# Optimization experiments

Hardware: AMD Instinct MI355X
Metric: run time of the kernel (lower is better)

Reference implementation:

```python
import jax, jax.numpy as jnp
import numpy as np

WS = 11
SIGMA = 1.5
CH = 3
C1 = (0.01 * 255.0) ** 2  # 6.5025
C2 = (0.03 * 255.0) ** 2  # 58.5225


def _gauss_window():
    # 1D Gaussian -> outer product -> depthwise kernel [C, 1, ws, ws] (OIHW)
    coords = jnp.arange(WS, dtype=jnp.float32) - WS // 2
    g = jnp.exp(-coords ** 2 / (2.0 * SIGMA ** 2))
    g = g / g.sum()
    w2d = g[:, None] * g[None, :]
    return jnp.tile(w2d[None, None], (CH, 1, 1, 1))


def _dwconv(x, win):
    pad = WS // 2
    return jax.lax.conv_general_dilated(
        x, win, window_strides=(1, 1), padding=[(pad, pad), (pad, pad)],
        feature_group_count=CH,
        dimension_numbers=('NCHW', 'OIHW', 'NCHW'))


def setup_inputs() -> dict:
    key = jax.random.key(0)
    k1, k2 = jax.random.split(key)
    shape = (32, 3, 512, 512)
    img_gen = jax.random.uniform(k1, shape, jnp.float32, -1.0, 1.0)
    img_ref = jax.random.uniform(k2, shape, jnp.float32, -1.0, 1.0)
    return {"img_gen": img_gen, "img_ref": img_ref}


def reference(img_gen, img_ref):
    gen = (img_gen + 1.0) * 0.5
    ref = (img_ref + 1.0) * 0.5
    win = _gauss_window()

    mu1 = _dwconv(gen, win)
    mu2 = _dwconv(ref, win)
    mu1_sq = mu1 * mu1
    mu2_sq = mu2 * mu2
    mu1_mu2 = mu1 * mu2
    sigma1_sq = _dwconv(gen * gen, win) - mu1_sq
    sigma2_sq = _dwconv(ref * ref, win) - mu2_sq
    sigma12 = _dwconv(gen * ref, win) - mu1_mu2

    ssim_map = ((2.0 * mu1_mu2 + C1) * (2.0 * sigma12 + C2)) / (
        (mu1_sq + mu2_sq + C1) * (sigma1_sq + sigma2_sq + C2))
    return 1.0 - ssim_map.mean()
```

## Files before the change

### kernel.cpp

```cpp
#include <hip/hip_runtime.h>

#define TX 64
#define TY 20
#define PROWS (TY + 10)
#define HSTR 67
#define IMW 512
#define IMH 512
#define NPLANES 96
#define NBX (IMW / TX)
#define NBY ((IMH + TY - 1) / TY)
#define NBLOCKS (NBX * NBY * NPLANES)

__device__ __forceinline__ float uniform_f(float v) {
  return __int_as_float(__builtin_amdgcn_readfirstlane(__float_as_int(v)));
}

__device__ __forceinline__ void gauss_weights(float* w) {
  double t[11];
  double s = 0.0;
#pragma unroll
  for (int i = 0; i < 11; ++i) {
    double d = (double)(i - 5);
    t[i] = exp(-d * d / 4.5);
    s += t[i];
  }
#pragma unroll
  for (int i = 0; i < 11; ++i) w[i] = uniform_f((float)(t[i] / s));
}

__global__ __launch_bounds__(256, 4) void ssim_main(
    const float* __restrict__ gen, const float* __restrict__ ref,
    float* __restrict__ partial) {
  __shared__ float sh[5][PROWS][HSTR];
  __shared__ float swsum[4];

  const int tid = threadIdx.x;
  const int bid = blockIdx.x;
  const int rem = bid % (NBX * NBY);
  const int plane = bid / (NBX * NBY);
  const int bx = rem % NBX;
  const int by = rem / NBX;
  const int x0 = bx * TX;
  const int y0 = by * TY;
  const float* gp = gen + (size_t)plane * (IMW * IMH);
  const float* rp = ref + (size_t)plane * (IMW * IMH);

  float w[11];
  gauss_weights(w);

  if (tid < PROWS * 8) {
    const int row = tid >> 3;
    const int xs = (tid & 7) * 8;
    const int gy = y0 - 5 + row;
    const bool rowok = (gy >= 0) && (gy < IMH);
    const int xbase = x0 + xs - 8;
    const float* grow = gp + (size_t)gy * IMW;
    const float* rrow = rp + (size_t)gy * IMW;

    float ga[24], ra[24];
#pragma unroll
    for (int k = 0; k < 6; ++k) {
      const int c = xbase + 4 * k;
      const bool ok = rowok && (c >= 0) && (c < IMW);
      float4 vg = make_float4(0.f, 0.f, 0.f, 0.f);
      float4 vr = make_float4(0.f, 0.f, 0.f, 0.f);
      if (ok) {
        float4 g4 = *(const float4*)(grow + c);
        float4 r4 = *(const float4*)(rrow + c);
        vg.x = fmaf(0.5f, g4.x, 0.5f); vg.y = fmaf(0.5f, g4.y, 0.5f);
        vg.z = fmaf(0.5f, g4.z, 0.5f); vg.w = fmaf(0.5f, g4.w, 0.5f);
        vr.x = fmaf(0.5f, r4.x, 0.5f); vr.y = fmaf(0.5f, r4.y, 0.5f);
        vr.z = fmaf(0.5f, r4.z, 0.5f); vr.w = fmaf(0.5f, r4.w, 0.5f);
      }
      ga[4 * k + 0] = vg.x; ga[4 * k + 1] = vg.y;
      ga[4 * k + 2] = vg.z; ga[4 * k + 3] = vg.w;
      ra[4 * k + 0] = vr.x; ra[4 * k + 1] = vr.y;
      ra[4 * k + 2] = vr.z; ra[4 * k + 3] = vr.w;
    }

    float acc[5][8];
#pragma unroll
    for (int q = 0; q < 5; ++q)
#pragma unroll
      for (int o = 0; o < 8; ++o) acc[q][o] = 0.f;

#pragma unroll
    for (int p = 0; p < 18; ++p) {
      const float g = ga[p + 3];
      const float r = ra[p + 3];
      const float gg = g * g;
      const float rr = r * r;
      const float gr = g * r;
      const int olo = (p - 10 < 0) ? 0 : p - 10;
      const int ohi = (p < 7) ? p : 7;
#pragma unroll
      for (int o = olo; o <= ohi; ++o) {
        const float wt = w[p - o];
        acc[0][o] = fmaf(wt, g, acc[0][o]);
        acc[1][o] = fmaf(wt, r, acc[1][o]);
        acc[2][o] = fmaf(wt, gg, acc[2][o]);
        acc[3][o] = fmaf(wt, rr, acc[3][o]);
        acc[4][o] = fmaf(wt, gr, acc[4][o]);
      }
    }
#pragma unroll
    for (int q = 0; q < 5; ++q)
#pragma unroll
      for (int o = 0; o < 8; ++o) sh[q][row][xs + o] = acc[q][o];
  }
  __syncthreads();

  const int col = tid & 63;
  const int r0 = (tid >> 6) * 5;
  float hv[5][15];
#pragma unroll
  for (int q = 0; q < 5; ++q)
#pragma unroll
    for (int i = 0; i < 15; ++i) hv[q][i] = sh[q][r0 + i][col];

  const float C1 = 6.5025f, C2 = 58.5225f;
  float lsum = 0.f;
#pragma unroll
  for (int o = 0; o < 5; ++o) {
    float mu1 = 0.f, mu2 = 0.f, e1 = 0.f, e2 = 0.f, e12 = 0.f;
#pragma unroll
    for (int t = 0; t < 11; ++t) {
      const float wt = w[t];
      mu1 = fmaf(wt, hv[0][o + t], mu1);
      mu2 = fmaf(wt, hv[1][o + t], mu2);
      e1 = fmaf(wt, hv[2][o + t], e1);
      e2 = fmaf(wt, hv[3][o + t], e2);
      e12 = fmaf(wt, hv[4][o + t], e12);
    }
    const float m12 = mu1 * mu2;
    const float m1s = mu1 * mu1;
    const float m2s = mu2 * mu2;
    const float num = (2.f * m12 + C1) * (2.f * (e12 - m12) + C2);
    const float den = (m1s + m2s + C1) * ((e1 - m1s) + (e2 - m2s) + C2);
    const int y = y0 + r0 + o;
    lsum += (y < IMH) ? (num / den) : 0.f;
  }

#pragma unroll
  for (int off = 32; off > 0; off >>= 1) lsum += __shfl_down(lsum, off, 64);
  if ((tid & 63) == 0) swsum[tid >> 6] = lsum;
  __syncthreads();
  if (tid == 0) partial[bid] = swsum[0] + swsum[1] + swsum[2] + swsum[3];
}

__global__ void ssim_reduce(const float* __restrict__ partial,
                            float* __restrict__ out) {
  const int nv = NBLOCKS / 4;
  double s = 0.0;
  for (int i = threadIdx.x; i < nv; i += 256) {
    float4 v = ((const float4*)partial)[i];
    s += (double)v.x + (double)v.y + (double)v.z + (double)v.w;
  }
#pragma unroll
  for (int off = 32; off > 0; off >>= 1) s += __shfl_down(s, off, 64);
  __shared__ double sd[4];
  if ((threadIdx.x & 63) == 0) sd[threadIdx.x >> 6] = s;
  __syncthreads();
  if (threadIdx.x == 0) {
    double npix = (double)NPLANES * (double)IMW * (double)IMH;
    out[0] = (float)(1.0 - (sd[0] + sd[1] + sd[2] + sd[3]) / npix);
  }
}

extern "C" void kernel_launch(void* const* d_in, const int* in_sizes, int n_in,
                              void* d_out, int out_size, void* d_ws, size_t ws_size,
                              hipStream_t stream) {
  (void)in_sizes; (void)n_in; (void)out_size; (void)ws_size;
  const float* gen = (const float*)d_in[0];
  const float* ref = (const float*)d_in[1];
  float* partial = (float*)d_ws;
  ssim_main<<<NBLOCKS, 256, 0, stream>>>(gen, ref, partial);
  ssim_reduce<<<1, 256, 0, stream>>>(partial, (float*)d_out);
}
```

Baseline: 310.5 us.

## Pack gen/ref channels into v_pk_fma_f32 and hardcode Gaussian weights

Pairs the gen and ref values (and their squares) into two-wide vectors and accumulates both blur passes with packed v_pk_fma_f32 inline asm, cutting the VALU instruction count for the separable convolution. It also hardcodes the Gaussian weights as constants instead of computing them in double precision per thread, adds a branch-free interior tile load path, reorganizes shared memory into interleaved float2 arrays written with float4 stores, and uses a fast divide. The risks are slightly different rounding from the fast divide and the constants, plus the inline asm limiting compiler scheduling. Out-of-bounds pixels now load -1 so they map to 0 after the affine transform.

```diff
diff --git a/kernel.cpp b/kernel.cpp
--- a/kernel.cpp
+++ b/kernel.cpp
@@ -1,9 +1,12 @@
 #include <hip/hip_runtime.h>
+
+typedef float v2f __attribute__((ext_vector_type(2)));
 
 #define TX 64
 #define TY 20
 #define PROWS (TY + 10)
-#define HSTR 67
+#define GRSTR 66
+#define SSTR 68
 #define IMW 512
 #define IMH 512
 #define NPLANES 96
@@ -11,28 +14,27 @@
 #define NBY ((IMH + TY - 1) / TY)
 #define NBLOCKS (NBX * NBY * NPLANES)
 
-__device__ __forceinline__ float uniform_f(float v) {
-  return __int_as_float(__builtin_amdgcn_readfirstlane(__float_as_int(v)));
-}
-
-__device__ __forceinline__ void gauss_weights(float* w) {
-  double t[11];
-  double s = 0.0;
-#pragma unroll
-  for (int i = 0; i < 11; ++i) {
-    double d = (double)(i - 5);
-    t[i] = exp(-d * d / 4.5);
-    s += t[i];
-  }
-#pragma unroll
-  for (int i = 0; i < 11; ++i) w[i] = uniform_f((float)(t[i] / s));
+#define GW0 0.00102838f
+#define GW1 0.00759877f
+#define GW2 0.03600077f
+#define GW3 0.10936069f
+#define GW4 0.21300553f
+#define GW5 0.26601172f
+
+__device__ __forceinline__ void pkfma(v2f& acc, v2f a, v2f b) {
+  asm("v_pk_fma_f32 %0, %1, %2, %0" : "+v"(acc) : "v"(a), "v"(b));
 }
 
 __global__ __launch_bounds__(256, 4) void ssim_main(
     const float* __restrict__ gen, const float* __restrict__ ref,
     float* __restrict__ partial) {
-  __shared__ float sh[5][PROWS][HSTR];
+  __shared__ __align__(16) v2f s_gr[PROWS][GRSTR];
+  __shared__ __align__(16) v2f s_qq[PROWS][GRSTR];
+  __shared__ __align__(16) float s_s[PROWS][SSTR];
   __shared__ float swsum[4];
+
+  const float GW[11] = {GW0, GW1, GW2, GW3, GW4, GW5,
+                        GW4, GW3, GW2, GW1, GW0};
 
   const int tid = threadIdx.x;
   const int bid = blockIdx.x;
@@ -45,100 +47,124 @@
   const float* gp = gen + (size_t)plane * (IMW * IMH);
   const float* rp = ref + (size_t)plane * (IMW * IMH);
 
-  float w[11];
-  gauss_weights(w);
-
   if (tid < PROWS * 8) {
     const int row = tid >> 3;
     const int xs = (tid & 7) * 8;
     const int gy = y0 - 5 + row;
-    const bool rowok = (gy >= 0) && (gy < IMH);
     const int xbase = x0 + xs - 8;
     const float* grow = gp + (size_t)gy * IMW;
     const float* rrow = rp + (size_t)gy * IMW;
 
-    float ga[24], ra[24];
-#pragma unroll
-    for (int k = 0; k < 6; ++k) {
-      const int c = xbase + 4 * k;
-      const bool ok = rowok && (c >= 0) && (c < IMW);
-      float4 vg = make_float4(0.f, 0.f, 0.f, 0.f);
-      float4 vr = make_float4(0.f, 0.f, 0.f, 0.f);
-      if (ok) {
-        float4 g4 = *(const float4*)(grow + c);
-        float4 r4 = *(const float4*)(rrow + c);
-        vg.x = fmaf(0.5f, g4.x, 0.5f); vg.y = fmaf(0.5f, g4.y, 0.5f);
-        vg.z = fmaf(0.5f, g4.z, 0.5f); vg.w = fmaf(0.5f, g4.w, 0.5f);
-        vr.x = fmaf(0.5f, r4.x, 0.5f); vr.y = fmaf(0.5f, r4.y, 0.5f);
-        vr.z = fmaf(0.5f, r4.z, 0.5f); vr.w = fmaf(0.5f, r4.w, 0.5f);
+    v2f P[24];
+    const bool interior = (bx >= 1) & (bx <= 6) & (by >= 1) & (by <= 24);
+    if (interior) {
+#pragma unroll
+      for (int k = 0; k < 6; ++k) {
+        const int c = xbase + 4 * k;
+        const float4 g4 = *(const float4*)(grow + c);
+        const float4 r4 = *(const float4*)(rrow + c);
+        P[4 * k + 0] = (v2f){fmaf(0.5f, g4.x, 0.5f), fmaf(0.5f, r4.x, 0.5f)};
+        P[4 * k + 1] = (v2f){fmaf(0.5f, g4.y, 0.5f), fmaf(0.5f, r4.y, 0.5f)};
+        P[4 * k + 2] = (v2f){fmaf(0.5f, g4.z, 0.5f), fmaf(0.5f, r4.z, 0.5f)};
+        P[4 * k + 3] = (v2f){fmaf(0.5f, g4.w, 0.5f), fmaf(0.5f, r4.w, 0.5f)};
       }
-      ga[4 * k + 0] = vg.x; ga[4 * k + 1] = vg.y;
-      ga[4 * k + 2] = vg.z; ga[4 * k + 3] = vg.w;
-      ra[4 * k + 0] = vr.x; ra[4 * k + 1] = vr.y;
-      ra[4 * k + 2] = vr.z; ra[4 * k + 3] = vr.w;
-    }
-
-    float acc[5][8];
-#pragma unroll
-    for (int q = 0; q < 5; ++q)
-#pragma unroll
-      for (int o = 0; o < 8; ++o) acc[q][o] = 0.f;
+    } else {
+      const bool rowok = (gy >= 0) && (gy < IMH);
+#pragma unroll
+      for (int k = 0; k < 6; ++k) {
+        const int c = xbase + 4 * k;
+        const bool ok = rowok && (c >= 0) && (c < IMW);
+        float4 g4 = make_float4(-1.f, -1.f, -1.f, -1.f);
+        float4 r4 = g4;
+        if (ok) {
+          g4 = *(const float4*)(grow + c);
+          r4 = *(const float4*)(rrow + c);
+        }
+        P[4 * k + 0] = (v2f){fmaf(0.5f, g4.x, 0.5f), fmaf(0.5f, r4.x, 0.5f)};
+        P[4 * k + 1] = (v2f){fmaf(0.5f, g4.y, 0.5f), fmaf(0.5f, r4.y, 0.5f)};
+        P[4 * k + 2] = (v2f){fmaf(0.5f, g4.z, 0.5f), fmaf(0.5f, r4.z, 0.5f)};
+        P[4 * k + 3] = (v2f){fmaf(0.5f, g4.w, 0.5f), fmaf(0.5f, r4.w, 0.5f)};
+      }
+    }
+
+    v2f accP[8], accQ[8];
+    float accS[8];
+#pragma unroll
+    for (int o = 0; o < 8; ++o) {
+      accP[o] = (v2f){0.f, 0.f};
+      accQ[o] = (v2f){0.f, 0.f};
+      accS[o] = 0.f;
+    }
 
 #pragma unroll
     for (int p = 0; p < 18; ++p) {
-      const float g = ga[p + 3];
-      const float r = ra[p + 3];
-      const float gg = g * g;
-      const float rr = r * r;
-      const float gr = g * r;
+      const v2f pv = P[p + 3];
+      v2f qv;
+      qv.x = pv.x * pv.x;
+      qv.y = pv.y * pv.y;
+      const float sv = pv.x * pv.y;
       const int olo = (p - 10 < 0) ? 0 : p - 10;
       const int ohi = (p < 7) ? p : 7;
 #pragma unroll
       for (int o = olo; o <= ohi; ++o) {
-        const float wt = w[p - o];
-        acc[0][o] = fmaf(wt, g, acc[0][o]);
-        acc[1][o] = fmaf(wt, r, acc[1][o]);
-        acc[2][o] = fmaf(wt, gg, acc[2][o]);
-        acc[3][o] = fmaf(wt, rr, acc[3][o]);
-        acc[4][o] = fmaf(wt, gr, acc[4][o]);
+        const float wt = GW[p - o];
+        const v2f wv = (v2f){wt, wt};
+        pkfma(accP[o], wv, pv);
+        pkfma(accQ[o], wv, qv);
+        accS[o] = fmaf(wt, sv, accS[o]);
       }
     }
-#pragma unroll
-    for (int q = 0; q < 5; ++q)
-#pragma unroll
-      for (int o = 0; o < 8; ++o) sh[q][row][xs + o] = acc[q][o];
+
+    float4* wp = (float4*)&s_gr[row][xs];
+    wp[0] = make_float4(accP[0].x, accP[0].y, accP[1].x, accP[1].y);
+    wp[1] = make_float4(accP[2].x, accP[2].y, accP[3].x, accP[3].y);
+    wp[2] = make_float4(accP[4].x, accP[4].y, accP[5].x, accP[5].y);
+    wp[3] = make_float4(accP[6].x, accP[6].y, accP[7].x, accP[7].y);
+    float4* wq = (float4*)&s_qq[row][xs];
+    wq[0] = make_float4(accQ[0].x, accQ[0].y, accQ[1].x, accQ[1].y);
+    wq[1] = make_float4(accQ[2].x, accQ[2].y, accQ[3].x, accQ[3].y);
+    wq[2] = make_float4(accQ[4].x, accQ[4].y, accQ[5].x, accQ[5].y);
+    wq[3] = make_float4(accQ[6].x, accQ[6].y, accQ[7].x, accQ[7].y);
+    float4* ws = (float4*)&s_s[row][xs];
+    ws[0] = make_float4(accS[0], accS[1], accS[2], accS[3]);
+    ws[1] = make_float4(accS[4], accS[5], accS[6], accS[7]);
   }
   __syncthreads();
 
   const int col = tid & 63;
   const int r0 = (tid >> 6) * 5;
-  float hv[5][15];
-#pragma unroll
-  for (int q = 0; q < 5; ++q)
-#pragma unroll
-    for (int i = 0; i < 15; ++i) hv[q][i] = sh[q][r0 + i][col];
+  v2f hp[15], hq[15];
+  float hs[15];
+#pragma unroll
+  for (int i = 0; i < 15; ++i) {
+    hp[i] = s_gr[r0 + i][col];
+    hq[i] = s_qq[r0 + i][col];
+    hs[i] = s_s[r0 + i][col];
+  }
 
   const float C1 = 6.5025f, C2 = 58.5225f;
   float lsum = 0.f;
 #pragma unroll
   for (int o = 0; o < 5; ++o) {
-    float mu1 = 0.f, mu2 = 0.f, e1 = 0.f, e2 = 0.f, e12 = 0.f;
+    v2f mu = (v2f){0.f, 0.f};
+    v2f ee = (v2f){0.f, 0.f};
+    float e12 = 0.f;
 #pragma unroll
     for (int t = 0; t < 11; ++t) {
-      const float wt = w[t];
-      mu1 = fmaf(wt, hv[0][o + t], mu1);
-      mu2 = fmaf(wt, hv[1][o + t], mu2);
-      e1 = fmaf(wt, hv[2][o + t], e1);
-      e2 = fmaf(wt, hv[3][o + t], e2);
-      e12 = fmaf(wt, hv[4][o + t], e12);
-    }
+      const float wt = GW[t];
+      const v2f wv = (v2f){wt, wt};
+      pkfma(mu, wv, hp[o + t]);
+      pkfma(ee, wv, hq[o + t]);
+      e12 = fmaf(wt, hs[o + t], e12);
+    }
+    const float mu1 = mu.x, mu2 = mu.y, e1 = ee.x, e2 = ee.y;
     const float m12 = mu1 * mu2;
     const float m1s = mu1 * mu1;
     const float m2s = mu2 * mu2;
     const float num = (2.f * m12 + C1) * (2.f * (e12 - m12) + C2);
     const float den = (m1s + m2s + C1) * ((e1 - m1s) + (e2 - m2s) + C2);
     const int y = y0 + r0 + o;
-    lsum += (y < IMH) ? (num / den) : 0.f;
+    lsum += (y < IMH) ? __fdividef(num, den) : 0.f;
   }
 
 #pragma unroll
```

Result: no change. 306.2 us (-1.4%).
